# Performance work log

Measured on AMD Instinct MI355X. Metric: run time of the kernel, lower is better.

The kernel has to match this reference:

```python
import jax, jax.numpy as jnp
import numpy as np

B, N, C, H, W = 32, 8, 256, 4, 4


def setup_inputs() -> dict:
    key = jax.random.key(0)
    k1, k2 = jax.random.split(key)
    pred = jax.random.normal(k1, (B, N, C, H, W), dtype=jnp.float32)
    gt = jax.random.normal(k2, (B, N, C, H, W), dtype=jnp.float32)
    return {"pred": pred, "gt": gt}


def reference(pred, gt):
    b, n, c, h, w = pred.shape
    M = b * n * h * w
    # (B,N,C,H,W) -> (B,N,H,W,C) -> (M, C)
    p = jnp.transpose(pred, (0, 1, 3, 4, 2)).reshape(M, c)
    # (B,N,C,H,W) -> (C,B,N,H,W) -> (C, M)
    g = jnp.transpose(gt, (2, 0, 1, 3, 4)).reshape(c, M)
    lossmat = p @ g  # (M, M) similarity matrix
    # CrossEntropy with target = arange(M): -mean(log_softmax diag)
    logp = jax.nn.log_softmax(lossmat, axis=1)
    loss = -jnp.mean(jnp.diagonal(logp))
    # accuracy (no grad in original)
    top1 = jnp.argmax(lossmat, axis=1)
    acc = jnp.mean((top1 == jnp.arange(M)).astype(jnp.float32)) * 100.0
    return (loss, acc)
```

## Files before the change

### kernel.cpp

```cpp
#include <hip/hip_runtime.h>
#include <cstdint>

typedef __bf16 bf16x8 __attribute__((ext_vector_type(8)));
typedef float floatx4 __attribute__((ext_vector_type(4)));


#define OFF_X     (0u)
#define OFF_Y     (2u*1024*1024)
#define OFF_PMAX  (4u*1024*1024)
#define OFF_PSUM  (5u*1024*1024)
#define OFF_DIAG  (6u*1024*1024)
#define OFF_LPART (OFF_DIAG + 16384u)
#define OFF_CPART (OFF_LPART + 256u)
#define OFF_CNT   (OFF_CPART + 256u)
#define OFF_SCR   (8u*1024*1024)

__global__ __launch_bounds__(256) void transpose_stage(
    const float* __restrict__ pred, const float* __restrict__ gt,
    unsigned short* __restrict__ Xs, unsigned short* __restrict__ Ys,
    int* __restrict__ cnt) {
  int blk = blockIdx.x;
  const int t = threadIdx.x;
  if (blk == 0 && t < 33) cnt[t] = 0;
  const float* src;
  unsigned short* dst;
  int slab;
  if (blk < 256) { src = pred; dst = Xs; slab = blk; }
  else           { src = gt;   dst = Ys; slab = blk - 256; }
  const float* sb = src + slab * 4096;
  const int rb = slab >> 3, rowhi = slab & 7;
  #pragma unroll
  for (int half = 0; half < 2; ++half) {
    int c_ = half * 256 + t;
    int rowlo = c_ & 15;
    int quad  = (c_ >> 4) & 3;
    int kk    = (c_ >> 6) & 1;
    int s     = c_ >> 7;
    int k0 = s * 64 + kk * 32 + quad * 8;
    unsigned int packed[4];
    #pragma unroll
    for (int jj = 0; jj < 4; ++jj) {
      unsigned int lohi[2];
      #pragma unroll
      for (int e = 0; e < 2; ++e) {
        float f = sb[(k0 + jj * 2 + e) * 16 + rowlo];
        unsigned int u = __float_as_uint(f);
        lohi[e] = (u + 0x7FFFu + ((u >> 16) & 1u)) >> 16;
      }
      packed[jj] = lohi[0] | (lohi[1] << 16);
    }
    unsigned short* o = dst + rb * 32768 +
        (unsigned)(s * 1024 + kk * 512 + rowhi * 64 + quad * 16 + rowlo) * 8;
    uint4 v; v.x = packed[0]; v.y = packed[1]; v.z = packed[2]; v.w = packed[3];
    *reinterpret_cast<uint4*>(o) = v;
  }
}

#define WAVE_MAP()                                                           \
  const int t = threadIdx.x;                                                 \
  const int wv = t >> 6, lane = t & 63;                                      \
  const int b = blockIdx.x;                                                  \
  const int xcd = b & 7, slot = b >> 3;                                      \
  const int rowb = ((xcd >> 1) << 4) | (slot & 15);                          \
  const int colb = ((xcd & 1) << 3) | (slot >> 4);                           \
  const int hh = rowb & 1, ch = wv & 1;                                      \
  const unsigned short* Ab = Xs + (rowb >> 1) * 32768 + (unsigned)lane * 8;  \
  const unsigned short* Bb = Ys + ((colb << 1) | (wv >> 1)) * 32768 +        \
                             (unsigned)lane * 8;

#define KOFF(KS) ((unsigned)((((KS) >> 1) * 1024 + ((KS)&1) * 512)) * 8)

#define LOADF(AR, BR, KS) do {                                               \
    _Pragma("unroll") for (int fr = 0; fr < 4; ++fr)                         \
      AR[fr] = *reinterpret_cast<const bf16x8*>(                             \
          Ab + KOFF(KS) + (unsigned)((hh * 4 + fr) * 64) * 8);               \
    _Pragma("unroll") for (int fc = 0; fc < 4; ++fc)                         \
      BR[fc] = *reinterpret_cast<const bf16x8*>(                             \
          Bb + KOFF(KS) + (unsigned)((ch * 4 + fc) * 64) * 8);               \
  } while (0)

#define MM(AR, BR) do {                                                      \
    _Pragma("unroll") for (int fr = 0; fr < 4; ++fr)                         \
      _Pragma("unroll") for (int fc = 0; fc < 4; ++fc)                       \
        acc[fr][fc] = __builtin_amdgcn_mfma_f32_16x16x32_bf16(               \
            AR[fr], BR[fc], acc[fr][fc], 0, 0, 0);                           \
  } while (0)

#define KLOOP_DBUF() do {                                                    \
    bf16x8 a0[4], b0[4], a1[4], b1[4];                                       \
    LOADF(a0, b0, 0);                                                        \
    LOADF(a1, b1, 1); MM(a0, b0);                                            \
    LOADF(a0, b0, 2); MM(a1, b1);                                            \
    LOADF(a1, b1, 3); MM(a0, b0);                                            \
    LOADF(a0, b0, 4); MM(a1, b1);                                            \
    LOADF(a1, b1, 5); MM(a0, b0);                                            \
    LOADF(a0, b0, 6); MM(a1, b1);                                            \
    LOADF(a1, b1, 7); MM(a0, b0);                                            \
    MM(a1, b1);                                                              \
  } while (0)

__global__ __launch_bounds__(256, 2) void gemm_wave2(
    const unsigned short* __restrict__ Xs, const unsigned short* __restrict__ Ys,
    float* __restrict__ pmax, float* __restrict__ psum, float* __restrict__ diag) {
  WAVE_MAP();
  floatx4 acc[4][4];
  const floatx4 zero = {0.f, 0.f, 0.f, 0.f};
  #pragma unroll
  for (int i = 0; i < 4; ++i)
    #pragma unroll
    for (int j = 0; j < 4; ++j) acc[i][j] = zero;

  KLOOP_DBUF();

  const int quad = lane >> 4, lc = lane & 15;

  if (colb * 4 + wv == rowb) {
    #pragma unroll
    for (int fr = 0; fr < 4; ++fr)
      #pragma unroll
      for (int r = 0; r < 4; ++r)
        if (lc == quad * 4 + r)
          diag[rowb * 64 + fr * 16 + lc] = acc[fr][fr][r];
  }

  #pragma unroll
  for (int fr = 0; fr < 4; ++fr) {
    #pragma unroll
    for (int r = 0; r < 4; ++r) {
      float v0 = acc[fr][0][r], v1 = acc[fr][1][r];
      float v2 = acc[fr][2][r], v3 = acc[fr][3][r];
      float m = fmaxf(fmaxf(v0, v1), fmaxf(v2, v3));
      #pragma unroll
      for (int sh = 1; sh < 16; sh <<= 1) m = fmaxf(m, __shfl_xor(m, sh, 64));
      float ss = __expf(v0 - m) + __expf(v1 - m) +
                 __expf(v2 - m) + __expf(v3 - m);
      #pragma unroll
      for (int sh = 1; sh < 16; sh <<= 1) ss += __shfl_xor(ss, sh, 64);
      if (lc == 0) {
        int grow = rowb * 64 + fr * 16 + quad * 4 + r;
        int p = grow * 64 + colb * 4 + wv;
        pmax[p] = m; psum[p] = ss;
      }
    }
  }
}

__global__ __launch_bounds__(256, 2) void probe_mfma(
    const unsigned short* __restrict__ Xs, const unsigned short* __restrict__ Ys,
    float* __restrict__ scratch) {
  WAVE_MAP();
  floatx4 acc[4][4];
  const floatx4 zero = {0.f, 0.f, 0.f, 0.f};
  #pragma unroll
  for (int i = 0; i < 4; ++i)
    #pragma unroll
    for (int j = 0; j < 4; ++j) acc[i][j] = zero;

  KLOOP_DBUF();

  floatx4 cs = zero;
  #pragma unroll
  for (int fr = 0; fr < 4; ++fr)
    #pragma unroll
    for (int fc = 0; fc < 4; ++fc) cs += acc[fr][fc];
  *reinterpret_cast<floatx4*>(scratch + (size_t)(b * 256 + t) * 4) = cs;
}

__global__ __launch_bounds__(256) void combine_rows(
    const float* __restrict__ pmax, const float* __restrict__ psum,
    const float* __restrict__ diag,
    float* __restrict__ lpart, float* __restrict__ cpart,
    int* __restrict__ cnt, float* __restrict__ out) {
  int row = blockIdx.x * 256 + threadIdx.x;
  const float* pm = pmax + row * 64;
  const float* ps = psum + row * 64;
  float M = -3.4e38f;
  #pragma unroll 8
  for (int b = 0; b < 64; ++b) M = fmaxf(M, pm[b]);
  float S = 0.f;
  #pragma unroll 8
  for (int b = 0; b < 64; ++b) S += ps[b] * __expf(pm[b] - M);
  float d = diag[row];
  float lossr = logf(S) + M - d;
  float corr = (d == M) ? 1.f : 0.f;
  #pragma unroll
  for (int sh = 1; sh < 64; sh <<= 1) {
    lossr += __shfl_xor(lossr, sh, 64);
    corr  += __shfl_xor(corr,  sh, 64);
  }
  __shared__ float ls[4], cs[4];
  int wave = threadIdx.x >> 6, lane = threadIdx.x & 63;
  if (lane == 0) { ls[wave] = lossr; cs[wave] = corr; }
  __syncthreads();
  if (threadIdx.x == 0) {
    lpart[blockIdx.x] = ls[0] + ls[1] + ls[2] + ls[3];
    cpart[blockIdx.x] = cs[0] + cs[1] + cs[2] + cs[3];
    __threadfence();
    if (atomicAdd(cnt, 1) == 15) {
      __threadfence();
      float L = 0.f, C = 0.f;
      for (int i = 0; i < 16; ++i) { L += lpart[i]; C += cpart[i]; }
      out[0] = L * (1.f / 4096.f);
      out[1] = C * (100.f / 4096.f);
    }
  }
}

extern "C" void kernel_launch(void* const* d_in, const int* in_sizes, int n_in,
                              void* d_out, int out_size, void* d_ws, size_t ws_size,
                              hipStream_t stream) {
  const float* pred = (const float*)d_in[0];
  const float* gt   = (const float*)d_in[1];
  char* w = (char*)d_ws;
  unsigned short* Xbf = (unsigned short*)(w + OFF_X);
  unsigned short* Ybf = (unsigned short*)(w + OFF_Y);
  float* pmax  = (float*)(w + OFF_PMAX);
  float* psum  = (float*)(w + OFF_PSUM);
  float* diag  = (float*)(w + OFF_DIAG);
  float* lpart = (float*)(w + OFF_LPART);
  float* cpart = (float*)(w + OFF_CPART);
  int*   cnt   = (int*)(w + OFF_CNT);
  float* scr   = (float*)(w + OFF_SCR);
  float* out   = (float*)d_out;

  transpose_stage<<<512, 256, 0, stream>>>(pred, gt, Xbf, Ybf, cnt);
  gemm_wave2<<<1024, 256, 0, stream>>>(Xbf, Ybf, pmax, psum, diag);
  combine_rows<<<16, 256, 0, stream>>>(pmax, psum, diag, lpart, cpart, cnt, out);
  probe_mfma<<<1024, 256, 0, stream>>>(Xbf, Ybf, scr);
}
```

Measured before the change: 101.4 us.

## Remove probe GEMM launch and assign tiles by hardware XCD via atomics

Drops the duplicate probe_mfma kernel, which recomputed the whole GEMM only to write scratch checksums. The main GEMM now reads the hardware XCC_ID register and claims a tile from that XCD's slot range through atomic counters. A spill path with atomicExch guarantees every tile is still claimed exactly once. This keeps tiles that share operand rows on the same XCD's L2 no matter how blocks are actually dispatched, at the cost of a few atomics and a barrier per block.

Result: no change. 103.0 us (+1.6%).

```diff
diff --git a/kernel.cpp b/kernel.cpp
--- a/kernel.cpp
+++ b/kernel.cpp
@@ -13,7 +13,6 @@
 #define OFF_LPART (OFF_DIAG + 16384u)
 #define OFF_CPART (OFF_LPART + 256u)
 #define OFF_CNT   (OFF_CPART + 256u)
-#define OFF_SCR   (8u*1024*1024)
 
 __global__ __launch_bounds__(256) void transpose_stage(
     const float* __restrict__ pred, const float* __restrict__ gt,
@@ -21,7 +20,9 @@
     int* __restrict__ cnt) {
   int blk = blockIdx.x;
   const int t = threadIdx.x;
-  if (blk == 0 && t < 33) cnt[t] = 0;
+  if (blk == 0) {
+    for (int i = t; i < 1088; i += 256) cnt[i] = 0;
+  }
   const float* src;
   unsigned short* dst;
   int slab;
@@ -55,18 +56,6 @@
     *reinterpret_cast<uint4*>(o) = v;
   }
 }
-
-#define WAVE_MAP()                                                           \
-  const int t = threadIdx.x;                                                 \
-  const int wv = t >> 6, lane = t & 63;                                      \
-  const int b = blockIdx.x;                                                  \
-  const int xcd = b & 7, slot = b >> 3;                                      \
-  const int rowb = ((xcd >> 1) << 4) | (slot & 15);                          \
-  const int colb = ((xcd & 1) << 3) | (slot >> 4);                           \
-  const int hh = rowb & 1, ch = wv & 1;                                      \
-  const unsigned short* Ab = Xs + (rowb >> 1) * 32768 + (unsigned)lane * 8;  \
-  const unsigned short* Bb = Ys + ((colb << 1) | (wv >> 1)) * 32768 +        \
-                             (unsigned)lane * 8;
 
 #define KOFF(KS) ((unsigned)((((KS) >> 1) * 1024 + ((KS)&1) * 512)) * 8)
 
@@ -99,10 +88,44 @@
     MM(a1, b1);                                                              \
   } while (0)
 
-__global__ __launch_bounds__(256, 2) void gemm_wave2(
+__global__ __launch_bounds__(256, 2) void gemm_wave3(
     const unsigned short* __restrict__ Xs, const unsigned short* __restrict__ Ys,
-    float* __restrict__ pmax, float* __restrict__ psum, float* __restrict__ diag) {
-  WAVE_MAP();
+    float* __restrict__ pmax, float* __restrict__ psum, float* __restrict__ diag,
+    int* __restrict__ cnt) {
+  const int t = threadIdx.x;
+  const int wv = t >> 6, lane = t & 63;
+
+  __shared__ int s_tile;
+  if (t == 0) {
+    unsigned x;
+    asm volatile("s_getreg_b32 %0, hwreg(HW_REG_XCC_ID)" : "=s"(x));
+    x &= 7u;
+    int* xslot = cnt + 1;
+    int* spill = cnt + 9;
+    int* claim = cnt + 64;
+    int s = atomicAdd(&xslot[x], 1);
+    int tile = -1;
+    if (s < 128) {
+      int cand = (int)(x * 128u + (unsigned)s);
+      if (atomicExch(&claim[cand], 1) == 0) tile = cand;
+    }
+    while (tile < 0) {
+      int o = atomicAdd(spill, 1) & 1023;
+      if (atomicExch(&claim[o], 1) == 0) tile = o;
+    }
+    s_tile = tile;
+  }
+  __syncthreads();
+  const int tile = s_tile;
+  const int xr = tile >> 7, local = tile & 127;
+  const int rowb = ((xr >> 1) << 4) | (local >> 3);
+  const int colb = ((xr & 1) << 3) | (local & 7);
+
+  const int hh = rowb & 1, ch = wv & 1;
+  const unsigned short* Ab = Xs + (rowb >> 1) * 32768 + (unsigned)lane * 8;
+  const unsigned short* Bb = Ys + ((colb << 1) | (wv >> 1)) * 32768 +
+                             (unsigned)lane * 8;
+
   floatx4 acc[4][4];
   const floatx4 zero = {0.f, 0.f, 0.f, 0.f};
   #pragma unroll
@@ -143,27 +166,6 @@
       }
     }
   }
-}
-
-__global__ __launch_bounds__(256, 2) void probe_mfma(
-    const unsigned short* __restrict__ Xs, const unsigned short* __restrict__ Ys,
-    float* __restrict__ scratch) {
-  WAVE_MAP();
-  floatx4 acc[4][4];
-  const floatx4 zero = {0.f, 0.f, 0.f, 0.f};
-  #pragma unroll
-  for (int i = 0; i < 4; ++i)
-    #pragma unroll
-    for (int j = 0; j < 4; ++j) acc[i][j] = zero;
-
-  KLOOP_DBUF();
-
-  floatx4 cs = zero;
-  #pragma unroll
-  for (int fr = 0; fr < 4; ++fr)
-    #pragma unroll
-    for (int fc = 0; fc < 4; ++fc) cs += acc[fr][fc];
-  *reinterpret_cast<floatx4*>(scratch + (size_t)(b * 256 + t) * 4) = cs;
 }
 
 __global__ __launch_bounds__(256) void combine_rows(
@@ -220,11 +222,9 @@
   float* lpart = (float*)(w + OFF_LPART);
   float* cpart = (float*)(w + OFF_CPART);
   int*   cnt   = (int*)(w + OFF_CNT);
-  float* scr   = (float*)(w + OFF_SCR);
   float* out   = (float*)d_out;
 
   transpose_stage<<<512, 256, 0, stream>>>(pred, gt, Xbf, Ybf, cnt);
-  gemm_wave2<<<1024, 256, 0, stream>>>(Xbf, Ybf, pmax, psum, diag);
+  gemm_wave3<<<1024, 256, 0, stream>>>(Xbf, Ybf, pmax, psum, diag, cnt);
   combine_rows<<<16, 256, 0, stream>>>(pmax, psum, diag, lpart, cpart, cnt, out);
-  probe_mfma<<<1024, 256, 0, stream>>>(Xbf, Ybf, scr);
-}
+}
```
